# Optimization experiments

Hardware: AMD Instinct MI355X
Metric: run time of the kernel (lower is better)

The kernel has to match this reference:

```python
import jax, jax.numpy as jnp
import numpy as np

U, B, D = 1024, 8, 512
H, HD = 8, 64
CL, RC = 64, 4            # chunk length, right-context per chunk
C = U // CL               # 16 chunks
R, S, M = C * RC, C, C - 1
Q, KV = R + U + S, M + R + U
PE = 2 * U - 1
NEG_INF = -1e8


def _chunk_mask():
    # True = disallowed connection. Query rows = [right_context(R), utterance(U), summary(S)];
    # key cols = [memory(M), right_context(R), utterance(U)].
    mask = np.ones((Q, KV), dtype=bool)
    for c in range(C):
        cols = []
        cols += list(range(0, c))                                  # memory of preceding chunks
        cols += list(range(M + c * RC, M + (c + 1) * RC))          # own right context
        u0 = max(0, c - 1) * CL                                    # one left-context chunk
        cols += list(range(M + R + u0, M + R + (c + 1) * CL))      # utterance up to own chunk
        cols = np.array(cols)
        rows = np.concatenate([
            np.arange(c * RC, (c + 1) * RC),                       # right-context queries
            np.arange(R + c * CL, R + (c + 1) * CL),               # utterance queries
            np.array([R + U + c]),                                 # summary query
        ])
        mask[np.ix_(rows, cols)] = False
    return jnp.asarray(mask)


def _xavier(key, shape):
    fan_in, fan_out = shape[-1], shape[0]
    a = (6.0 / (fan_in + fan_out)) ** 0.5
    return jax.random.uniform(key, shape, jnp.float32, -a, a)


def setup_inputs() -> dict:
    key = jax.random.key(0)
    ks = jax.random.split(key, 16)
    return {
        "utterance": jax.random.normal(ks[0], (U, B, D), jnp.float32),
        "lengths": jax.random.randint(ks[1], (B,), U // 2, U + 1),
        "right_context": jax.random.normal(ks[2], (R, B, D), jnp.float32),
        "summary": jax.random.normal(ks[3], (S, B, D), jnp.float32),
        "memory": jax.random.normal(ks[4], (M, B, D), jnp.float32),
        "attention_mask": _chunk_mask(),
        "pos_emb": jax.random.normal(ks[5], (PE, D), jnp.float32),
        "W_kv": _xavier(ks[6], (2 * D, D)),
        "b_kv": jnp.zeros((2 * D,), jnp.float32),
        "W_q": _xavier(ks[7], (D, D)),
        "b_q": jnp.zeros((D,), jnp.float32),
        "W_out": _xavier(ks[8], (D, D)),
        "b_out": jnp.zeros((D,), jnp.float32),
        "W_pos": _xavier(ks[9], (D, D)),
        "pos_bias_u": _xavier(ks[10], (H, HD)),
        "pos_bias_v": _xavier(ks[11], (H, HD)),
    }


def reference(utterance, lengths, right_context, summary, memory, attention_mask,
              pos_emb, W_kv, b_kv, W_q, b_q, W_out, b_out, W_pos,
              pos_bias_u, pos_bias_v):
    u_len, b, d = utterance.shape
    r, m, s = right_context.shape[0], memory.shape[0], summary.shape[0]
    h = pos_bias_u.shape[0]
    hd = d // h
    scaling = hd ** -0.5

    query = jnp.concatenate([right_context, utterance, summary], 0) @ W_q.T + b_q   # (Q,B,D)
    kv = jnp.concatenate([memory, right_context, utterance], 0) @ W_kv.T + b_kv     # (KV,B,2D)
    key_t, val_t = kv[..., :d], kv[..., d:]
    q_len, kv_len = query.shape[0], key_t.shape[0]

    k = key_t.reshape(kv_len, b, h, hd).transpose(1, 2, 0, 3)   # (B,H,KV,hd)
    v = val_t.reshape(kv_len, b, h, hd).transpose(1, 2, 0, 3)   # (B,H,KV,hd)
    q = query.reshape(q_len, b, h, hd)                           # (Q,B,H,hd)

    qu = (q + pos_bias_u).transpose(1, 2, 0, 3)                  # (B,H,Q,hd)
    matrix_ac = jnp.einsum('bhqe,bhke->bhqk', qu, k)             # (B,H,Q,KV)

    qv = (q[r:r + u_len] + pos_bias_v).transpose(1, 2, 0, 3)     # (B,H,U,hd)
    pe_len = pos_emb.shape[0]
    pos = (pos_emb @ W_pos.T).reshape(pe_len, h, hd).transpose(1, 0, 2)  # (H,PE,hd)
    bd_u = jnp.einsum('bhue,hpe->bhup', qv, pos)                 # (B,H,U,PE)

    # rel_shift: out[u, j] = in[u, U-1-u+j]
    out_len = pe_len - (u_len - 1)
    idx = (u_len - 1) - jnp.arange(u_len)[:, None] + jnp.arange(out_len)[None, :]
    bd_u = jnp.take_along_axis(bd_u, idx[None, None], axis=-1)   # (B,H,U,out_len)

    matrix_bd = jnp.zeros_like(matrix_ac).at[:, :, r:r + u_len, m + r:].set(bd_u)
    w = (matrix_ac + matrix_bd) * scaling

    w = jnp.where(attention_mask[None, None], NEG_INF, w)
    pad = jnp.arange(kv_len)[None, :] >= (kv_len - u_len + lengths)[:, None]  # (B,KV)
    w = jnp.where(pad[:, None, None, :], NEG_INF, w)

    probs = jax.nn.softmax(w, axis=-1)
    attn = jnp.einsum('bhqk,bhke->bhqe', probs, v)               # (B,H,Q,hd)
    attn = attn.transpose(2, 0, 1, 3).reshape(q_len, b, d)       # (Q,B,D)

    out_ru = attn[:r + u_len] @ W_out.T + b_out                  # (R+U,B,D)
    out_mem = jnp.clip(attn[r + u_len:], -10.0, 10.0)            # (S,B,D); tanh_on_mem=False
    return out_ru, out_mem
```

## Files before the change

kernel.cpp:

```cpp
#include <hip/hip_runtime.h>
#include <hip/hip_bf16.h>

typedef __hip_bfloat16 bf16;
typedef __attribute__((ext_vector_type(8))) short short8v;
typedef __attribute__((ext_vector_type(4))) float float4v;

#define UU 1024
#define BB 8
#define DD 512
#define HH 8
#define HD 64
#define RR 64
#define SS 16
#define MM 15
#define QQ 1104
#define KVL 1103
#define PEL 2047
#define NU 1536
#define MU 8952

#define AS1 __attribute__((address_space(1)))
#define AS3 __attribute__((address_space(3)))

__device__ __forceinline__ float lo16(unsigned u) { return __uint_as_float(u << 16); }
__device__ __forceinline__ float hi16(unsigned u) { return __uint_as_float(u & 0xffff0000u); }
__device__ __forceinline__ unsigned pk2(float a, float b) {
  unsigned short x = __builtin_bit_cast(unsigned short, __float2bfloat16(a));
  unsigned short y = __builtin_bit_cast(unsigned short, __float2bfloat16(b));
  return (unsigned)x | ((unsigned)y << 16);
}

struct PackDesc {
  const void* src[16];
  unsigned int srcoff[16];
  unsigned int dstoff[16];
  unsigned int cum[17];
};

__global__ __launch_bounds__(256) void pack_all(PackDesc d, bf16* base,
                                                const void* __restrict__ probe,
                                                int* __restrict__ flagout,
                                                int nchunks) {
  __shared__ int wsum[4];
  const unsigned short* p = (const unsigned short*)probe;
  int big = 0;
  for (int i = threadIdx.x; i < 4096; i += 256)
    big += (((p[i] >> 7) & 0xFF) >= 137) ? 1 : 0;
  #pragma unroll
  for (int off = 32; off; off >>= 1) big += __shfl_down(big, off);
  if ((threadIdx.x & 63) == 0) wsum[threadIdx.x >> 6] = big;
  __syncthreads();
  const int flag = (wsum[0] + wsum[1] + wsum[2] + wsum[3] < 16) ? 1 : 0;
  if (threadIdx.x == 0 && blockIdx.x == 0) *flagout = flag;

  int g = blockIdx.x * 256 + threadIdx.x;
  if (g >= nchunks) return;
  int s = 0;
  #pragma unroll
  for (int i = 1; i < 17; ++i) s += (g >= d.cum[i]) ? 1 : 0;
  unsigned local = (g - d.cum[s]) * 8u;
  bf16* dst = base + d.dstoff[s] + local;
  if (flag) {
    const uint4 v = *(const uint4*)((const bf16*)d.src[s] + d.srcoff[s] + local);
    *(uint4*)dst = v;
  } else {
    const float* fp = (const float*)d.src[s] + d.srcoff[s] + local;
    uint4 o;
    o.x = pk2(fp[0], fp[1]);
    o.y = pk2(fp[2], fp[3]);
    o.z = pk2(fp[4], fp[5]);
    o.w = pk2(fp[6], fp[7]);
    *(uint4*)dst = o;
  }
}

struct GemmP {
  const bf16* X; const bf16* W; const bf16* bias; void* out;
  int M, N, K; const int* outf;
};

__global__ __launch_bounds__(256) void gemm_dual(GemmP g0, GemmP g1, int ysplit) {
  __shared__ bf16 As[128 * 128];
  __shared__ bf16 Bs[128 * 128];
  GemmP g; int bm, bn;
  if ((int)blockIdx.y < ysplit) {
    g = g0; bm = blockIdx.y * 128; bn = blockIdx.x * 128;
  } else {
    g = g1;
    int nt = g1.N >> 7;
    int bi = ((int)blockIdx.y - ysplit) * gridDim.x + blockIdx.x;
    if (bi >= ((g1.M + 127) >> 7) * nt) return;
    bm = (bi / nt) * 128; bn = (bi % nt) * 128;
  }
  const int tid = threadIdx.x;
  const int lane = tid & 63, wv = tid >> 6;
  const int wr = wv >> 1, wc = wv & 1;
  const int l4 = lane >> 4;
  const int lb = lane & 15;
  const int quad = lane >> 4, l15 = lane & 15;

  float4v acc[4][4] = {};

  for (int kb = 0; kb < g.K; kb += 128) {
    #pragma unroll
    for (int i = 0; i < 8; ++i) {
      int r = wv * 32 + i * 4 + l4;
      int gm = bm + r; if (gm > g.M - 1) gm = g.M - 1;
      const bf16* src = g.X + (size_t)gm * g.K + kb + ((lb ^ (r & 15)) * 8);
      __builtin_amdgcn_global_load_lds((const AS1 void*)src,
                                       (AS3 void*)&As[(wv * 32 + i * 4) * 128], 16, 0, 0);
    }
    #pragma unroll
    for (int i = 0; i < 8; ++i) {
      int r = wv * 32 + i * 4 + l4;
      int gn = bn + r; if (gn > g.N - 1) gn = g.N - 1;
      const bf16* src = g.W + (size_t)gn * g.K + kb + ((lb ^ (r & 15)) * 8);
      __builtin_amdgcn_global_load_lds((const AS1 void*)src,
                                       (AS3 void*)&Bs[(wv * 32 + i * 4) * 128], 16, 0, 0);
    }
    __syncthreads();
    #pragma unroll
    for (int ki = 0; ki < 4; ++ki) {
      const int gblk = ki * 4 + quad;
      const int slot = (gblk ^ l15) * 8;
      short8v a[4], bq[4];
      #pragma unroll
      for (int t = 0; t < 4; ++t) {
        a[t]  = *(const short8v*)&As[(wr * 64 + t * 16 + l15) * 128 + slot];
        bq[t] = *(const short8v*)&Bs[(wc * 64 + t * 16 + l15) * 128 + slot];
      }
      #pragma unroll
      for (int mt = 0; mt < 4; ++mt)
        #pragma unroll
        for (int nt = 0; nt < 4; ++nt)
          acc[mt][nt] = __builtin_amdgcn_mfma_f32_16x16x32_bf16(
              a[mt], bq[nt], acc[mt][nt], 0, 0, 0);
    }
    __syncthreads();
  }

  const bool as_bf16 = (g.outf == nullptr) ? true : (*g.outf != 0);
  #pragma unroll
  for (int mt = 0; mt < 4; ++mt) {
    #pragma unroll
    for (int r = 0; r < 4; ++r) {
      int gm = bm + wr * 64 + mt * 16 + quad * 4 + r;
      if (gm >= g.M) continue;
      #pragma unroll
      for (int nt = 0; nt < 4; ++nt) {
        int gn = bn + wc * 64 + nt * 16 + l15;
        float v = acc[mt][nt][r];
        if (g.bias) v += __bfloat162float(g.bias[gn]);
        size_t o = (size_t)gm * g.N + gn;
        if (as_bf16) ((bf16*)g.out)[o] = __float2bfloat16(v);
        else         ((float*)g.out)[o] = v;
      }
    }
  }
}

__device__ __forceinline__ int gcol(int row, int c, int u0, int ncols) {
  if (row < c) return row;
  if (row < c + 4) return 15 + 4 * c + (row - c);
  if (row < ncols) return 79 + u0 + (row - c - 4);
  return 0;
}

__global__ __launch_bounds__(256, 2) void attn_chunk(
    const bf16* __restrict__ qkv, const bf16* __restrict__ pos,
    const bf16* __restrict__ pbu, const bf16* __restrict__ pbv,
    const int* __restrict__ lengths, bf16* __restrict__ attn,
    const int* __restrict__ flag, void* __restrict__ dout) {
  __shared__ char lds[65536];
  bf16* Vs   = (bf16*)(lds);
  bf16* Aqu  = (bf16*)(lds + 19456);
  bf16* Kt   = (bf16*)(lds + 29696);
  bf16* Aqv  = (bf16*)(lds + 32768);
  bf16* Psl  = (bf16*)(lds + 40960);
  bf16* Eb   = (bf16*)(lds + 49152);
  bf16* Pp   = (bf16*)(lds + 19456);
  float* wred  = (float*)(lds + 46336);
  float* rstat = (float*)(lds + 47616);

  const int idx = blockIdx.x;
  const int h = idx & 7, b = (idx >> 3) & 7, c = idx >> 6;
  const int u0 = c ? (c - 1) * 64 : 0;
  const int nut = c ? 128 : 64;
  const int ncols = c + 4 + nut;
  const int q0 = c ? 63 : 127;
  const int tid = threadIdx.x, lane = tid & 63, wv = tid >> 6;
  const int quad = lane >> 4, l15 = lane & 15, key = l15 & 7;
  const int lenlim = lengths[b] - u0;
  const bool obf = (*flag != 0);

  {
    int lr = lane >> 3;
    int sbr = (lane & 7) ^ lr;
    for (int i = wv; i < 19; i += 4) {
      int row = i * 8 + lr;
      int g = gcol(row, c, u0, ncols);
      int sbv = (lane & 7) ^ (i & 7);
      const bf16* src = qkv + ((size_t)(g * 8 + b)) * NU + 1024 + h * 64 + sbv * 8;
      __builtin_amdgcn_global_load_lds((const AS1 void*)src, (AS3 void*)(Vs + i * 512), 16, 0, 0);
    }
    for (int i = wv; i < 24; i += 4) {
      int p = i * 8 + lr;
      const bf16* src = pos + (size_t)p * 512 + h * 64 + sbr * 8;
      __builtin_amdgcn_global_load_lds((const AS1 void*)src, (AS3 void*)(Psl + i * 512), 16, 0, 0);
    }
  }
  for (int id = tid; id < 1152; id += 256) {
    bool isv = id >= 640;
    int lid = isv ? id - 640 : id;
    int m = lid >> 3, ec = lid & 7;
    int qrow;
    if (isv) qrow = 64 + 64 * c + m;
    else qrow = (m < 64) ? (64 + 64 * c + m)
              : (m < 68) ? (4 * c + (m - 64))
              : (m == 68) ? (1088 + c) : 0;
    const uint4 qa = *(const uint4*)(qkv + ((size_t)((qrow + 15) * 8 + b)) * NU + h * 64 + ec * 8);
    const uint4 ba = *(const uint4*)((isv ? pbv : pbu) + h * 64 + ec * 8);
    uint4 o;
    o.x = pk2(lo16(qa.x) + lo16(ba.x), hi16(qa.x) + hi16(ba.x));
    o.y = pk2(lo16(qa.y) + lo16(ba.y), hi16(qa.y) + hi16(ba.y));
    o.z = pk2(lo16(qa.z) + lo16(ba.z), hi16(qa.z) + hi16(ba.z));
    o.w = pk2(lo16(qa.w) + lo16(ba.w), hi16(qa.w) + hi16(ba.w));
    *(uint4*)((isv ? Aqv : Aqu) + m * 64 + (ec ^ (m & 7)) * 8) = o;
  }
  __syncthreads();

  float4v eacc[4][3];
  #pragma unroll
  for (int mt = 0; mt < 4; ++mt)
    #pragma unroll
    for (int i = 0; i < 3; ++i) eacc[mt][i] = (float4v){0.f, 0.f, 0.f, 0.f};
  {
    short8v av[4][2];
    #pragma unroll
    for (int mt = 0; mt < 4; ++mt)
      #pragma unroll
      for (int ks = 0; ks < 2; ++ks)
        av[mt][ks] = *(const short8v*)&Aqv[(mt * 16 + l15) * 64 + ((ks * 4 + quad) ^ key) * 8];
    #pragma unroll
    for (int nti = 0; nti < 3; ++nti) {
      int nt = wv + nti * 4;
      short8v b0 = *(const short8v*)&Psl[(nt * 16 + l15) * 64 + (quad ^ key) * 8];
      short8v b1 = *(const short8v*)&Psl[(nt * 16 + l15) * 64 + ((4 + quad) ^ key) * 8];
      #pragma unroll
      for (int mt = 0; mt < 4; ++mt) {
        eacc[mt][nti] = __builtin_amdgcn_mfma_f32_16x16x32_bf16(av[mt][0], b0, eacc[mt][nti], 0, 0, 0);
        eacc[mt][nti] = __builtin_amdgcn_mfma_f32_16x16x32_bf16(av[mt][1], b1, eacc[mt][nti], 0, 0, 0);
      }
    }
  }
  __syncthreads();

  {
    int lr = lane >> 3, sbr = (lane & 7) ^ lr;
    for (int i = wv; i < 19; i += 4) {
      int row = i * 8 + lr;
      int g = gcol(row, c, u0, ncols);
      const bf16* src = qkv + ((size_t)(g * 8 + b)) * NU + 512 + h * 64 + sbr * 8;
      __builtin_amdgcn_global_load_lds((const AS1 void*)src, (AS3 void*)(Kt + i * 512), 16, 0, 0);
    }
  }
  #pragma unroll
  for (int nti = 0; nti < 3; ++nti) {
    int p = (wv + nti * 4) * 16 + l15;
    #pragma unroll
    for (int mt = 0; mt < 4; ++mt)
      #pragma unroll
      for (int r = 0; r < 4; ++r) {
        int m = mt * 16 + quad * 4 + r;
        int jl = p - q0 + m;
        if (jl >= 0 && jl < nut)
          Eb[m * 128 + (jl ^ (((m >> 2) & 7) << 4))] = __float2bfloat16(eacc[mt][nti][r]);
      }
  }
  __syncthreads();

  const int nnt = (wv < 2) ? 3 : 2;
  float4v sacc[5][3];
  #pragma unroll
  for (int mt = 0; mt < 5; ++mt)
    #pragma unroll
    for (int i = 0; i < 3; ++i) sacc[mt][i] = (float4v){0.f, 0.f, 0.f, 0.f};
  {
    short8v au[5][2];
    #pragma unroll
    for (int mt = 0; mt < 5; ++mt)
      #pragma unroll
      for (int ks = 0; ks < 2; ++ks)
        au[mt][ks] = *(const short8v*)&Aqu[(mt * 16 + l15) * 64 + ((ks * 4 + quad) ^ key) * 8];
    #pragma unroll
    for (int nti = 0; nti < 3; ++nti) {
      if (nti < nnt) {
        int nt = wv + nti * 4;
        short8v b0 = *(const short8v*)&Kt[(nt * 16 + l15) * 64 + (quad ^ key) * 8];
        short8v b1 = *(const short8v*)&Kt[(nt * 16 + l15) * 64 + ((4 + quad) ^ key) * 8];
        #pragma unroll
        for (int mt = 0; mt < 5; ++mt) {
          sacc[mt][nti] = __builtin_amdgcn_mfma_f32_16x16x32_bf16(au[mt][0], b0, sacc[mt][nti], 0, 0, 0);
          sacc[mt][nti] = __builtin_amdgcn_mfma_f32_16x16x32_bf16(au[mt][1], b1, sacc[mt][nti], 0, 0, 0);
        }
      }
    }
  }
  __syncthreads();

  #pragma unroll
  for (int nti = 0; nti < 3; ++nti) {
    if (nti < nnt) {
      int colv = (wv + nti * 4) * 16 + l15;
      int jl = colv - (c + 4);
      bool cvalid = (colv < ncols) && !(jl >= 0 && jl >= lenlim);
      #pragma unroll
      for (int mt = 0; mt < 5; ++mt)
        #pragma unroll
        for (int r = 0; r < 4; ++r) {
          float s = sacc[mt][nti][r];
          if (cvalid) {
            if (mt < 4 && jl >= 0) {
              int m = mt * 16 + quad * 4 + r;
              s += __bfloat162float(Eb[m * 128 + (jl ^ (((m >> 2) & 7) << 4))]);
            }
            s *= 0.125f;
          } else s = -1e30f;
          sacc[mt][nti][r] = s;
        }
    }
  }

  {
    #pragma unroll
    for (int mt = 0; mt < 5; ++mt)
      #pragma unroll
      for (int r = 0; r < 4; ++r) {
        float v = -3e38f;
        #pragma unroll
        for (int nti = 0; nti < 3; ++nti)
          if (nti < nnt) v = fmaxf(v, sacc[mt][nti][r]);
        v = fmaxf(v, __shfl_xor(v, 1));
        v = fmaxf(v, __shfl_xor(v, 2));
        v = fmaxf(v, __shfl_xor(v, 4));
        v = fmaxf(v, __shfl_xor(v, 8));
        if (l15 == 0) wred[(mt * 16 + quad * 4 + r) * 4 + wv] = v;
      }
  }
  __syncthreads();
  if (tid < 80)
    rstat[tid] = fmaxf(fmaxf(wred[tid * 4], wred[tid * 4 + 1]),
                       fmaxf(wred[tid * 4 + 2], wred[tid * 4 + 3]));
  __syncthreads();

  {
    float rmx[5][4], rsum[5][4];
    #pragma unroll
    for (int mt = 0; mt < 5; ++mt)
      #pragma unroll
      for (int r = 0; r < 4; ++r) {
        rmx[mt][r] = rstat[mt * 16 + quad * 4 + r];
        rsum[mt][r] = 0.f;
      }
    #pragma unroll
    for (int nti = 0; nti < 3; ++nti) {
      if (nti < nnt) {
        int colv = (wv + nti * 4) * 16 + l15;
        #pragma unroll
        for (int mt = 0; mt < 5; ++mt)
          #pragma unroll
          for (int r = 0; r < 4; ++r) {
            float p = __expf(sacc[mt][nti][r] - rmx[mt][r]);
            Pp[(mt * 16 + quad * 4 + r) * 168 + colv] = __float2bfloat16(p);
            rsum[mt][r] += p;
          }
      }
    }
    #pragma unroll
    for (int mt = 0; mt < 5; ++mt)
      #pragma unroll
      for (int r = 0; r < 4; ++r) {
        float v = rsum[mt][r];
        v += __shfl_xor(v, 1);
        v += __shfl_xor(v, 2);
        v += __shfl_xor(v, 4);
        v += __shfl_xor(v, 8);
        if (l15 == 0) wred[(mt * 16 + quad * 4 + r) * 4 + wv] = v;
      }
  }
  __syncthreads();
  if (tid < 80)
    rstat[tid] = 1.f / (wred[tid * 4] + wred[tid * 4 + 1] + wred[tid * 4 + 2] + wred[tid * 4 + 3]);
  __syncthreads();

  const int kmax = (ncols + 31) >> 5;
  float4v oacc[5];
  #pragma unroll
  for (int mt = 0; mt < 5; ++mt) oacc[mt] = (float4v){0.f, 0.f, 0.f, 0.f};
  const int ehi = (wv * 16 + l15) >> 3, elo = l15 & 7;
  for (int ks = 0; ks < kmax; ++ks) {
    short8v bq;
    const int blk = ehi ^ ((ks * 4 + quad) & 7);
    #pragma unroll
    for (int j = 0; j < 8; ++j)
      bq[j] = ((const short*)Vs)[(ks * 32 + quad * 8 + j) * 64 + blk * 8 + elo];
    #pragma unroll
    for (int mt = 0; mt < 5; ++mt) {
      short8v af = *(const short8v*)&Pp[(mt * 16 + l15) * 168 + ks * 32 + quad * 8];
      oacc[mt] = __builtin_amdgcn_mfma_f32_16x16x32_bf16(af, bq, oacc[mt], 0, 0, 0);
    }
  }

  #pragma unroll
  for (int mt = 0; mt < 5; ++mt) {
    #pragma unroll
    for (int r = 0; r < 4; ++r) {
      int m = mt * 16 + quad * 4 + r;
      if (m >= 69) continue;
      float o = oacc[mt][r] * rstat[m];
      if (m < 68) {
        int qrow = (m < 64) ? (64 + 64 * c + m) : (4 * c + (m - 64));
        attn[((size_t)(qrow * 8 + b)) * 512 + h * 64 + wv * 16 + l15] = __float2bfloat16(o);
      } else {
        float v = fminf(fmaxf(o, -10.f), 10.f);
        size_t oi = (size_t)1088 * 8 * 512 + ((size_t)(c * 8 + b)) * 512 + h * 64 + wv * 16 + l15;
        if (obf) ((bf16*)dout)[oi] = __float2bfloat16(v);
        else     ((float*)dout)[oi] = v;
      }
    }
  }
}

static inline int cdiv(int a, int b) { return (a + b - 1) / b; }

extern "C" void kernel_launch(void* const* d_in, const int* in_sizes, int n_in,
                              void* d_out, int out_size, void* d_ws, size_t ws_size,
                              hipStream_t stream) {
  const void* utter = d_in[0];
  const int*  lens  = (const int*)d_in[1];
  const void* rctx  = d_in[2];
  const void* summ  = d_in[3];
  const void* memry = d_in[4];
  const void* pose  = d_in[6];
  const void* W_kv  = d_in[7];
  const void* b_kv  = d_in[8];
  const void* W_q   = d_in[9];
  const void* b_q   = d_in[10];
  const void* W_out = d_in[11];
  const void* b_out = d_in[12];
  const void* W_pos = d_in[13];
  const void* pbu   = d_in[14];
  const void* pbv   = d_in[15];

  const unsigned SZ_MM = MM * BB * DD;
  const unsigned SZ_RC = RR * BB * DD;
  const unsigned SZ_UT = UU * BB * DD;
  const unsigned SZ_SM = SS * BB * DD;
  const unsigned N_XU  = SZ_MM + SZ_RC + SZ_UT + SZ_SM;
  const unsigned SZ_PS = 191 * DD;

  int*  flag = (int*)d_ws;
  bf16* base = (bf16*)((char*)d_ws + 64);
  unsigned off = 0;
  bf16* XU    = base + off; unsigned o_XU    = off; off += N_XU;
  bf16* posec = base + off; unsigned o_posec = off; off += 192 * DD;
  bf16* Wcat  = base + off; unsigned o_Wcat  = off; off += (unsigned)NU * DD;
  bf16* bcat  = base + off; unsigned o_bcat  = off; off += NU;
  bf16* Wout  = base + off; unsigned o_Wout  = off; off += DD * DD;
  bf16* bout  = base + off; unsigned o_bout  = off; off += DD;
  bf16* Wpos  = base + off; unsigned o_Wpos  = off; off += DD * DD;
  bf16* pbuc  = base + off; unsigned o_pbu   = off; off += DD;
  bf16* pbvc  = base + off; unsigned o_pbv   = off; off += DD;
  bf16* qkv   = base + off; off += (unsigned)(MU + 8) * NU;
  bf16* pos   = base + off; off += 192 * DD;
  bf16* attn  = base + off; off += QQ * BB * DD;

  PackDesc pd;
  const void* srcs[14]  = {memry, rctx, utter, summ, pose,
                           W_q, W_kv, b_q, b_kv, W_out, b_out, W_pos, pbu, pbv};
  unsigned    soffs[14] = {0, 0, 0, 0, 896u * DD, 0, 0, 0, 0, 0, 0, 0, 0, 0};
  unsigned    doffs[14] = {o_XU, o_XU + SZ_MM, o_XU + SZ_MM + SZ_RC,
                           o_XU + SZ_MM + SZ_RC + SZ_UT, o_posec,
                           o_Wcat, o_Wcat + DD * DD, o_bcat, o_bcat + DD,
                           o_Wout, o_bout, o_Wpos, o_pbu, o_pbv};
  unsigned    ns[14]    = {SZ_MM, SZ_RC, SZ_UT, SZ_SM, SZ_PS,
                           DD * DD, 2 * DD * DD, DD, 2 * DD,
                           DD * DD, DD, DD * DD, DD, DD};
  unsigned cum = 0;
  for (int i = 0; i < 14; ++i) {
    pd.src[i] = srcs[i]; pd.srcoff[i] = soffs[i]; pd.dstoff[i] = doffs[i];
    pd.cum[i] = cum; cum += ns[i] / 8;
  }
  pd.src[14] = pbv; pd.srcoff[14] = 0; pd.dstoff[14] = o_pbv;
  pd.src[15] = pbv; pd.srcoff[15] = 0; pd.dstoff[15] = o_pbv;
  pd.cum[14] = cum; pd.cum[15] = cum; pd.cum[16] = cum;
  int nchunks = (int)cum;
  pack_all<<<dim3(cdiv(nchunks, 256)), dim3(256), 0, stream>>>(pd, base, utter, flag, nchunks);

  GemmP gq{XU, Wcat, bcat, qkv, MU, NU, DD, nullptr};
  GemmP gp{posec, Wpos, nullptr, pos, 191, DD, DD, nullptr};
  gemm_dual<<<dim3(12, 71), dim3(256), 0, stream>>>(gq, gp, 70);

  attn_chunk<<<dim3(1024), dim3(256), 0, stream>>>(qkv, pos, pbuc, pbvc, lens, attn,
                                                   flag, d_out);

  GemmP go{attn, Wout, bout, d_out, (RR + UU) * BB, DD, DD, flag};
  gemm_dual<<<dim3(4, 68), dim3(256), 0, stream>>>(go, go, 68);
}
```

Baseline: 220.8 us.

## Read bf16 inputs directly in GEMMs and shrink GEMM row tile to 64

```diff
diff --git a/kernel.cpp b/kernel.cpp
--- a/kernel.cpp
+++ b/kernel.cpp
@@ -52,6 +52,7 @@
   __syncthreads();
   const int flag = (wsum[0] + wsum[1] + wsum[2] + wsum[3] < 16) ? 1 : 0;
   if (threadIdx.x == 0 && blockIdx.x == 0) *flagout = flag;
+  if (flag) return;
 
   int g = blockIdx.x * 256 + threadIdx.x;
   if (g >= nchunks) return;
@@ -60,77 +61,85 @@
   for (int i = 1; i < 17; ++i) s += (g >= d.cum[i]) ? 1 : 0;
   unsigned local = (g - d.cum[s]) * 8u;
   bf16* dst = base + d.dstoff[s] + local;
-  if (flag) {
-    const uint4 v = *(const uint4*)((const bf16*)d.src[s] + d.srcoff[s] + local);
-    *(uint4*)dst = v;
-  } else {
-    const float* fp = (const float*)d.src[s] + d.srcoff[s] + local;
-    uint4 o;
-    o.x = pk2(fp[0], fp[1]);
-    o.y = pk2(fp[2], fp[3]);
-    o.z = pk2(fp[4], fp[5]);
-    o.w = pk2(fp[6], fp[7]);
-    *(uint4*)dst = o;
-  }
+  const float* fp = (const float*)d.src[s] + d.srcoff[s] + local;
+  uint4 o;
+  o.x = pk2(fp[0], fp[1]);
+  o.y = pk2(fp[2], fp[3]);
+  o.z = pk2(fp[4], fp[5]);
+  o.w = pk2(fp[6], fp[7]);
+  *(uint4*)dst = o;
 }
 
 struct GemmP {
-  const bf16* X; const bf16* W; const bf16* bias; void* out;
-  int M, N, K; const int* outf;
+  const bf16* xo[4]; const bf16* xp[4]; int xlim[4]; int xbase[4];
+  const bf16* wo[2]; const bf16* wp[2]; int wlim0; int wbase1;
+  const bf16* bo[2]; const bf16* bp[2]; int hasbias;
+  void* out; int M, N, K; int oflag;
 };
 
-__global__ __launch_bounds__(256) void gemm_dual(GemmP g0, GemmP g1, int ysplit) {
-  __shared__ bf16 As[128 * 128];
+__global__ __launch_bounds__(256) void gemm_dual(GemmP g0, GemmP g1, int ysplit,
+                                                 const int* __restrict__ flag) {
+  __shared__ bf16 As[64 * 128];
   __shared__ bf16 Bs[128 * 128];
+  const bool bf = (*flag != 0);
   GemmP g; int bm, bn;
   if ((int)blockIdx.y < ysplit) {
-    g = g0; bm = blockIdx.y * 128; bn = blockIdx.x * 128;
+    g = g0; bm = blockIdx.y * 64; bn = blockIdx.x * 128;
   } else {
     g = g1;
     int nt = g1.N >> 7;
     int bi = ((int)blockIdx.y - ysplit) * gridDim.x + blockIdx.x;
-    if (bi >= ((g1.M + 127) >> 7) * nt) return;
-    bm = (bi / nt) * 128; bn = (bi % nt) * 128;
-  }
+    if (bi >= ((g1.M + 63) >> 6) * nt) return;
+    bm = (bi / nt) * 64; bn = (bi % nt) * 128;
+  }
+  const bf16* xs[4];
+  #pragma unroll
+  for (int i = 0; i < 4; ++i) xs[i] = bf ? g.xo[i] : g.xp[i];
+  const bf16* w0 = bf ? g.wo[0] : g.wp[0];
+  const bf16* w1 = bf ? g.wo[1] : g.wp[1];
+
   const int tid = threadIdx.x;
   const int lane = tid & 63, wv = tid >> 6;
   const int wr = wv >> 1, wc = wv & 1;
-  const int l4 = lane >> 4;
+  const int lr4 = lane >> 4;
   const int lb = lane & 15;
   const int quad = lane >> 4, l15 = lane & 15;
 
-  float4v acc[4][4] = {};
+  float4v acc[2][4] = {};
 
   for (int kb = 0; kb < g.K; kb += 128) {
     #pragma unroll
+    for (int i = 0; i < 4; ++i) {
+      int r = wv * 16 + i * 4 + lr4;
+      int gm = bm + r; if (gm > g.M - 1) gm = g.M - 1;
+      int s = (gm >= g.xlim[0]) + (gm >= g.xlim[1]) + (gm >= g.xlim[2]);
+      const bf16* src = xs[s] + (size_t)(gm - g.xbase[s]) * g.K + kb + ((lb ^ (r & 15)) * 8);
+      __builtin_amdgcn_global_load_lds((const AS1 void*)src,
+                                       (AS3 void*)&As[(wv * 16 + i * 4) * 128], 16, 0, 0);
+    }
+    #pragma unroll
     for (int i = 0; i < 8; ++i) {
-      int r = wv * 32 + i * 4 + l4;
-      int gm = bm + r; if (gm > g.M - 1) gm = g.M - 1;
-      const bf16* src = g.X + (size_t)gm * g.K + kb + ((lb ^ (r & 15)) * 8);
-      __builtin_amdgcn_global_load_lds((const AS1 void*)src,
-                                       (AS3 void*)&As[(wv * 32 + i * 4) * 128], 16, 0, 0);
-    }
-    #pragma unroll
-    for (int i = 0; i < 8; ++i) {
-      int r = wv * 32 + i * 4 + l4;
+      int r = wv * 32 + i * 4 + lr4;
       int gn = bn + r; if (gn > g.N - 1) gn = g.N - 1;
-      const bf16* src = g.W + (size_t)gn * g.K + kb + ((lb ^ (r & 15)) * 8);
+      const bf16* src = ((gn < g.wlim0) ? w0 + (size_t)gn * g.K
+                                        : w1 + (size_t)(gn - g.wbase1) * g.K)
+                        + kb + ((lb ^ (r & 15)) * 8);
       __builtin_amdgcn_global_load_lds((const AS1 void*)src,
                                        (AS3 void*)&Bs[(wv * 32 + i * 4) * 128], 16, 0, 0);
     }
     __syncthreads();
     #pragma unroll
     for (int ki = 0; ki < 4; ++ki) {
-      const int gblk = ki * 4 + quad;
-      const int slot = (gblk ^ l15) * 8;
-      short8v a[4], bq[4];
-      #pragma unroll
-      for (int t = 0; t < 4; ++t) {
-        a[t]  = *(const short8v*)&As[(wr * 64 + t * 16 + l15) * 128 + slot];
+      const int slot = ((ki * 4 + quad) ^ l15) * 8;
+      short8v a[2], bq[4];
+      #pragma unroll
+      for (int t = 0; t < 2; ++t)
+        a[t] = *(const short8v*)&As[(wr * 32 + t * 16 + l15) * 128 + slot];
+      #pragma unroll
+      for (int t = 0; t < 4; ++t)
         bq[t] = *(const short8v*)&Bs[(wc * 64 + t * 16 + l15) * 128 + slot];
-      }
-      #pragma unroll
-      for (int mt = 0; mt < 4; ++mt)
+      #pragma unroll
+      for (int mt = 0; mt < 2; ++mt)
         #pragma unroll
         for (int nt = 0; nt < 4; ++nt)
           acc[mt][nt] = __builtin_amdgcn_mfma_f32_16x16x32_bf16(
@@ -139,18 +148,21 @@
     __syncthreads();
   }
 
-  const bool as_bf16 = (g.outf == nullptr) ? true : (*g.outf != 0);
-  #pragma unroll
-  for (int mt = 0; mt < 4; ++mt) {
+  const bool as_bf16 = g.oflag ? bf : true;
+  const bf16* b0 = bf ? g.bo[0] : g.bp[0];
+  const bf16* b1 = bf ? g.bo[1] : g.bp[1];
+  #pragma unroll
+  for (int mt = 0; mt < 2; ++mt) {
     #pragma unroll
     for (int r = 0; r < 4; ++r) {
-      int gm = bm + wr * 64 + mt * 16 + quad * 4 + r;
+      int gm = bm + wr * 32 + mt * 16 + quad * 4 + r;
       if (gm >= g.M) continue;
       #pragma unroll
       for (int nt = 0; nt < 4; ++nt) {
         int gn = bn + wc * 64 + nt * 16 + l15;
         float v = acc[mt][nt][r];
-        if (g.bias) v += __bfloat162float(g.bias[gn]);
+        if (g.hasbias)
+          v += __bfloat162float((gn < g.wlim0) ? b0[gn] : b1[gn - g.wbase1]);
         size_t o = (size_t)gm * g.N + gn;
         if (as_bf16) ((bf16*)g.out)[o] = __float2bfloat16(v);
         else         ((float*)g.out)[o] = v;
@@ -168,7 +180,8 @@
 
 __global__ __launch_bounds__(256, 2) void attn_chunk(
     const bf16* __restrict__ qkv, const bf16* __restrict__ pos,
-    const bf16* __restrict__ pbu, const bf16* __restrict__ pbv,
+    const bf16* __restrict__ pbu_o, const bf16* __restrict__ pbu_p,
+    const bf16* __restrict__ pbv_o, const bf16* __restrict__ pbv_p,
     const int* __restrict__ lengths, bf16* __restrict__ attn,
     const int* __restrict__ flag, void* __restrict__ dout) {
   __shared__ char lds[65536];
@@ -192,6 +205,8 @@
   const int quad = lane >> 4, l15 = lane & 15, key = l15 & 7;
   const int lenlim = lengths[b] - u0;
   const bool obf = (*flag != 0);
+  const bf16* pbu = obf ? pbu_o : pbu_p;
+  const bf16* pbv = obf ? pbv_o : pbv_p;
 
   {
     int lr = lane >> 3;
@@ -466,9 +481,9 @@
   bf16* posec = base + off; unsigned o_posec = off; off += 192 * DD;
   bf16* Wcat  = base + off; unsigned o_Wcat  = off; off += (unsigned)NU * DD;
   bf16* bcat  = base + off; unsigned o_bcat  = off; off += NU;
-  bf16* Wout  = base + off; unsigned o_Wout  = off; off += DD * DD;
-  bf16* bout  = base + off; unsigned o_bout  = off; off += DD;
-  bf16* Wpos  = base + off; unsigned o_Wpos  = off; off += DD * DD;
+  bf16* Woutp = base + off; unsigned o_Wout  = off; off += DD * DD;
+  bf16* boutp = base + off; unsigned o_bout  = off; off += DD;
+  bf16* Wposp = base + off; unsigned o_Wpos  = off; off += DD * DD;
   bf16* pbuc  = base + off; unsigned o_pbu   = off; off += DD;
   bf16* pbvc  = base + off; unsigned o_pbv   = off; off += DD;
   bf16* qkv   = base + off; off += (unsigned)(MU + 8) * NU;
@@ -497,13 +512,50 @@
   int nchunks = (int)cum;
   pack_all<<<dim3(cdiv(nchunks, 256)), dim3(256), 0, stream>>>(pd, base, utter, flag, nchunks);
 
-  GemmP gq{XU, Wcat, bcat, qkv, MU, NU, DD, nullptr};
-  GemmP gp{posec, Wpos, nullptr, pos, 191, DD, DD, nullptr};
-  gemm_dual<<<dim3(12, 71), dim3(256), 0, stream>>>(gq, gp, 70);
-
-  attn_chunk<<<dim3(1024), dim3(256), 0, stream>>>(qkv, pos, pbuc, pbvc, lens, attn,
-                                                   flag, d_out);
-
-  GemmP go{attn, Wout, bout, d_out, (RR + UU) * BB, DD, DD, flag};
-  gemm_dual<<<dim3(4, 68), dim3(256), 0, stream>>>(go, go, 68);
+  const int BIG = 1 << 30;
+  GemmP gq;
+  gq.xo[0] = (const bf16*)memry; gq.xo[1] = (const bf16*)rctx;
+  gq.xo[2] = (const bf16*)utter; gq.xo[3] = (const bf16*)summ;
+  gq.xp[0] = XU; gq.xp[1] = XU + SZ_MM; gq.xp[2] = XU + SZ_MM + SZ_RC;
+  gq.xp[3] = XU + SZ_MM + SZ_RC + SZ_UT;
+  gq.xlim[0] = 120; gq.xlim[1] = 632; gq.xlim[2] = 8824; gq.xlim[3] = BIG;
+  gq.xbase[0] = 0; gq.xbase[1] = 120; gq.xbase[2] = 632; gq.xbase[3] = 8824;
+  gq.wo[0] = (const bf16*)W_q; gq.wo[1] = (const bf16*)W_kv;
+  gq.wp[0] = Wcat; gq.wp[1] = Wcat + DD * DD;
+  gq.wlim0 = 512; gq.wbase1 = 512;
+  gq.bo[0] = (const bf16*)b_q; gq.bo[1] = (const bf16*)b_kv;
+  gq.bp[0] = bcat; gq.bp[1] = bcat + DD;
+  gq.hasbias = 1; gq.out = qkv; gq.M = MU; gq.N = NU; gq.K = DD; gq.oflag = 0;
+
+  GemmP gp;
+  gp.xo[0] = (const bf16*)pose + (size_t)896 * DD; gp.xp[0] = posec;
+  gp.xo[1] = gp.xo[0]; gp.xp[1] = posec; gp.xo[2] = gp.xo[0]; gp.xp[2] = posec;
+  gp.xo[3] = gp.xo[0]; gp.xp[3] = posec;
+  gp.xlim[0] = BIG; gp.xlim[1] = BIG; gp.xlim[2] = BIG; gp.xlim[3] = BIG;
+  gp.xbase[0] = 0; gp.xbase[1] = 0; gp.xbase[2] = 0; gp.xbase[3] = 0;
+  gp.wo[0] = (const bf16*)W_pos; gp.wo[1] = (const bf16*)W_pos;
+  gp.wp[0] = Wposp; gp.wp[1] = Wposp;
+  gp.wlim0 = BIG; gp.wbase1 = 0;
+  gp.bo[0] = gp.bo[1] = nullptr; gp.bp[0] = gp.bp[1] = nullptr;
+  gp.hasbias = 0; gp.out = pos; gp.M = 191; gp.N = DD; gp.K = DD; gp.oflag = 0;
+
+  gemm_dual<<<dim3(12, 141), dim3(256), 0, stream>>>(gq, gp, 140, flag);
+
+  attn_chunk<<<dim3(1024), dim3(256), 0, stream>>>(
+      qkv, pos, (const bf16*)pbu, pbuc, (const bf16*)pbv, pbvc, lens, attn, flag, d_out);
+
+  GemmP go;
+  go.xo[0] = attn; go.xp[0] = attn;
+  go.xo[1] = attn; go.xp[1] = attn; go.xo[2] = attn; go.xp[2] = attn;
+  go.xo[3] = attn; go.xp[3] = attn;
+  go.xlim[0] = BIG; go.xlim[1] = BIG; go.xlim[2] = BIG; go.xlim[3] = BIG;
+  go.xbase[0] = 0; go.xbase[1] = 0; go.xbase[2] = 0; go.xbase[3] = 0;
+  go.wo[0] = (const bf16*)W_out; go.wo[1] = (const bf16*)W_out;
+  go.wp[0] = Woutp; go.wp[1] = Woutp;
+  go.wlim0 = BIG; go.wbase1 = 0;
+  go.bo[0] = (const bf16*)b_out; go.bo[1] = (const bf16*)b_out;
+  go.bp[0] = boutp; go.bp[1] = boutp;
+  go.hasbias = 1; go.out = d_out; go.M = (RR + UU) * BB; go.N = DD; go.K = DD;
+  go.oflag = 1;
+  gemm_dual<<<dim3(4, 136), dim3(256), 0, stream>>>(go, go, 136, flag);
 }
```

Result: slower. 268.5 us (+21.6%).
